# Kernel optimization log

Measured on AMD Instinct MI355X. Metric: run time of the kernel, lower is better.

The kernel has to match this reference:

```python
import jax, jax.numpy as jnp
import numpy as np

S, B, D, H, L = 512, 64, 512, 512, 2


def setup_inputs() -> dict:
    key = jax.random.key(0)
    ks = jax.random.split(key, 2 + 4 * L * 2)
    x = jax.random.normal(ks[0], (S, B, D), jnp.float32)
    # ragged lengths -> time-major float mask, as the torch module expects
    lengths = jax.random.randint(ks[1], (B,), S // 2, S + 1)
    mask = (jnp.arange(S)[:, None] < lengths[None, :]).astype(jnp.float32)
    inp = {"x": x, "mask": mask}
    s = 1.0 / np.sqrt(H)  # torch RNNCell default init scale
    ki = 2
    for l in range(L):
        in_dim = D if l == 0 else 2 * H
        for d in ("f", "b"):
            k1, k2, k3, k4 = jax.random.split(ks[ki], 4)
            ki += 1
            inp[f"Wih{l}{d}"] = jax.random.uniform(k1, (4 * H, in_dim), jnp.float32, -s, s)
            inp[f"Whh{l}{d}"] = jax.random.uniform(k2, (4 * H, H), jnp.float32, -s, s)
            inp[f"bih{l}{d}"] = jax.random.uniform(k3, (4 * H,), jnp.float32, -s, s)
            inp[f"bhh{l}{d}"] = jax.random.uniform(k4, (4 * H,), jnp.float32, -s, s)
    return inp


def _run_lstm(x, mask, Wih, Whh, bih, bhh, reverse):
    # x: [S,B,in], mask: [S,B]. init hidden is zeros (init_hidden=None path),
    # so the mask blend h*m + h0*(1-m) reduces to h*m.
    b = x.shape[1]
    h0 = jnp.zeros((b, H), x.dtype)

    def step(carry, inp):
        xt, mt = inp
        h, c = carry
        gates = xt @ Wih.T + bih + h @ Whh.T + bhh  # [B, 4H]
        i, f, g, o = jnp.split(gates, 4, axis=-1)
        c2 = jax.nn.sigmoid(f) * c + jax.nn.sigmoid(i) * jnp.tanh(g)
        h2 = jax.nn.sigmoid(o) * jnp.tanh(c2)
        m = mt[:, None]
        h2 = h2 * m
        c2 = c2 * m
        return (h2, c2), h2

    (hn, cn), out = jax.lax.scan(step, (h0, h0), (x, mask), reverse=reverse)
    return out, hn, cn


def reference(x, mask,
              Wih0f, Whh0f, bih0f, bhh0f, Wih0b, Whh0b, bih0b, bhh0b,
              Wih1f, Whh1f, bih1f, bhh1f, Wih1b, Whh1b, bih1b, bhh1b):
    layers = [((Wih0f, Whh0f, bih0f, bhh0f), (Wih0b, Whh0b, bih0b, bhh0b)),
              ((Wih1f, Whh1f, bih1f, bhh1f), (Wih1b, Whh1b, bih1b, bhh1b))]
    h = x
    hn, cn = [], []
    for pf, pb in layers:
        of, hf, cf = _run_lstm(h, mask, *pf, reverse=False)
        ob, hb, cb = _run_lstm(h, mask, *pb, reverse=True)
        h = jnp.concatenate([of, ob], axis=2)  # [S,B,2H]
        hn.append(jnp.concatenate([hf, hb], axis=1))
        cn.append(jnp.concatenate([cf, cb], axis=1))
    return h, (jnp.stack(hn, axis=0), jnp.stack(cn, axis=0))
```

## Files before the change

### kernel.cpp

```cpp
#include <hip/hip_runtime.h>
#include <hip/hip_bf16.h>
#include <stdint.h>

#define S_LEN 512
#define BATCH 64
#define DDIM  512
#define HID   512
#define SB    32768

typedef __attribute__((ext_vector_type(8))) short bf16x8;
typedef __attribute__((ext_vector_type(4))) short short4v;
typedef __attribute__((ext_vector_type(4))) float f32x4;

struct __align__(128) Bar { unsigned cnt; unsigned gen; };

__device__ __forceinline__ float bf2f(short s) {
  return __uint_as_float(((unsigned)(unsigned short)s) << 16);
}

__device__ __forceinline__ void gload_lds16(const void* g, void* l) {
  __builtin_amdgcn_global_load_lds(
      (const __attribute__((address_space(1))) void*)g,
      (__attribute__((address_space(3))) void*)l, 16, 0, 0);
}


__global__ void k_f32_to_bf16(const float* __restrict__ src,
                              __hip_bfloat16* __restrict__ dst, int n) {
  int i = (blockIdx.x * blockDim.x + threadIdx.x) * 8;
  if (i >= n) return;
  float4 a = *(const float4*)(src + i);
  float4 b = *(const float4*)(src + i + 4);
  __hip_bfloat16 t[8];
  t[0] = __float2bfloat16(a.x); t[1] = __float2bfloat16(a.y);
  t[2] = __float2bfloat16(a.z); t[3] = __float2bfloat16(a.w);
  t[4] = __float2bfloat16(b.x); t[5] = __float2bfloat16(b.y);
  t[6] = __float2bfloat16(b.z); t[7] = __float2bfloat16(b.w);
  *(bf16x8*)(dst + i) = *(bf16x8*)t;
}

__global__ void k_permW(const float* __restrict__ src,
                        __hip_bfloat16* __restrict__ dst, int K) {
  int idx = blockIdx.x * 256 + threadIdx.x;
  int p = idx / K, k = idx - p * K;
  int g = p & 3, j = p >> 2;
  dst[idx] = __float2bfloat16(src[(size_t)(g * HID + j) * K + k]);
}

__global__ void k_permB(const float* __restrict__ bih, const float* __restrict__ bhh,
                        float* __restrict__ dst) {
  int p = blockIdx.x * 256 + threadIdx.x;
  int g = p & 3, j = p >> 2;
  dst[p] = bih[g * HID + j] + bhh[g * HID + j];
}

__global__ __launch_bounds__(256) void k_gemm_in(
    const __hip_bfloat16* __restrict__ A,
    const __hip_bfloat16* __restrict__ W,
    const float* __restrict__ bsumL,
    __hip_bfloat16* __restrict__ G,
    int K) {
  __shared__ uint4 lds4[2048];
  char* ldsA = (char*)lds4;
  char* ldsB = (char*)lds4 + 16384;
  int tid = threadIdx.x, lane = tid & 63, wid = tid >> 6;
  int wm = wid >> 1, wn = wid & 1;
  int bm = blockIdx.x, by = blockIdx.y;
  int lr = lane & 15, lk = lane >> 4;
  f32x4 acc[4][4] = {};
  const char* gA = (const char*)A;
  const char* gW = (const char*)W;
  for (int kk = 0; kk < K; kk += 64) {
    #pragma unroll
    for (int i = 0; i < 4; i++) {
      int ch = i * 256 + tid;
      int row = ch >> 3, c16 = ch & 7;
      gload_lds16(gA + (size_t)(bm * 128 + row) * (K * 2) + kk * 2 + c16 * 16,
                  ldsA + (i * 256 + wid * 64) * 16);
      gload_lds16(gW + (size_t)(by * 128 + row) * (K * 2) + kk * 2 + c16 * 16,
                  ldsB + (i * 256 + wid * 64) * 16);
    }
    __syncthreads();
    #pragma unroll
    for (int ks = 0; ks < 2; ks++) {
      bf16x8 af[4], bfr[4];
      #pragma unroll
      for (int mi = 0; mi < 4; mi++) {
        int r = wm * 64 + mi * 16 + lr;
        af[mi] = *(const bf16x8*)(ldsA + r * 128 + ks * 64 + lk * 16);
      }
      #pragma unroll
      for (int ni = 0; ni < 4; ni++) {
        int r = wn * 64 + ni * 16 + lr;
        bfr[ni] = *(const bf16x8*)(ldsB + r * 128 + ks * 64 + lk * 16);
      }
      #pragma unroll
      for (int mi = 0; mi < 4; mi++)
        #pragma unroll
        for (int ni = 0; ni < 4; ni++)
          acc[mi][ni] = __builtin_amdgcn_mfma_f32_16x16x32_bf16(
              af[mi], bfr[ni], acc[mi][ni], 0, 0, 0);
    }
    __syncthreads();
  }
  #pragma unroll
  for (int ni = 0; ni < 4; ni++) {
    int n = by * 128 + wn * 64 + ni * 16 + lr;
    int d = n >> 11, p = n & 2047;
    float bias = bsumL[d * 2048 + p];
    #pragma unroll
    for (int mi = 0; mi < 4; mi++) {
      int mbase = bm * 128 + wm * 64 + mi * 16 + lk * 4;
      #pragma unroll
      for (int r = 0; r < 4; r++) {
        int m = mbase + r;
        G[((size_t)d * SB + m) * 2048 + p] =
            __float2bfloat16(acc[mi][ni][r] + bias);
      }
    }
  }
}

__global__ __launch_bounds__(512, 1) void k_scan(
    const __hip_bfloat16* __restrict__ G,
    const __hip_bfloat16* __restrict__ Whp,
    __hip_bfloat16* __restrict__ Y,
    const float* __restrict__ mask,
    float* __restrict__ outH,
    float* __restrict__ hn, float* __restrict__ cn,
    Bar* __restrict__ bars) {
  __shared__ char ldsH[65536];
  float* gatesF = (float*)ldsH;
  int tid = threadIdx.x, lane = tid & 63, wid = tid >> 6;
  int bn = blockIdx.x & 31;
  int dir = blockIdx.x >> 5;
  int wm = wid >> 1, wn = wid & 1;
  int lr = lane & 15, lk = lane >> 4;
  int arow = wm * 16 + lr;
  Bar* bar = bars + dir;
  const __hip_bfloat16* Gd = G + (size_t)dir * SB * 2048;

  int cb = tid >> 3, cup = tid & 7;

  bf16x8 bfrag[16][2];
  {
    const __hip_bfloat16* w0 =
        Whp + (size_t)(dir * 2048 + bn * 64 + wn * 32 + lr) * 512;
    #pragma unroll
    for (int ni = 0; ni < 2; ni++)
      #pragma unroll
      for (int ks = 0; ks < 16; ks++)
        bfrag[ks][ni] = *(const bf16x8*)(w0 + (size_t)ni * 16 * 512 + ks * 32 + lk * 8);
  }

  float creg[2] = {0.f, 0.f};

  int t0 = dir ? (S_LEN - 1) : 0;
  bf16x8 gv = *(const bf16x8*)(Gd + ((size_t)t0 * 64 + cb) * 2048 + bn * 64 + cup * 8);

  for (int s = 0; s < S_LEN; ++s) {
    int t = dir ? (S_LEN - 1 - s) : s;
    f32x4 acc[2] = {};
    if (s > 0) {
      int tprev = dir ? t + 1 : t - 1;
      const char* srcH = (const char*)Y + (size_t)tprev * 131072 + dir * 1024;
      uint64_t tH[16];
      #pragma unroll
      for (int i = 0; i < 16; ++i) {
        int ch = i * 512 + tid, row = ch >> 7, c8 = ch & 127;
        tH[i] = __hip_atomic_load(
            (const uint64_t*)(srcH + (size_t)row * 2048 + c8 * 8),
            __ATOMIC_RELAXED, __HIP_MEMORY_SCOPE_AGENT);
      }
      #pragma unroll
      for (int i = 0; i < 16; ++i) {
        int ch = i * 512 + tid, row = ch >> 7, c8 = ch & 127;
        *(uint64_t*)(ldsH + row * 1024 + ((c8 * 8) ^ ((row & 7) << 4))) = tH[i];
      }
      __syncthreads();
      #pragma unroll
      for (int ks = 0; ks < 16; ++ks) {
        bf16x8 a = *(const bf16x8*)(
            ldsH + arow * 1024 + ((ks * 64 + lk * 16) ^ ((arow & 7) << 4)));
        acc[0] = __builtin_amdgcn_mfma_f32_16x16x32_bf16(a, bfrag[ks][0], acc[0], 0, 0, 0);
        acc[1] = __builtin_amdgcn_mfma_f32_16x16x32_bf16(a, bfrag[ks][1], acc[1], 0, 0, 0);
      }
      __syncthreads();
      #pragma unroll
      for (int ni = 0; ni < 2; ++ni)
        #pragma unroll
        for (int r = 0; r < 4; ++r)
          gatesF[(wm * 16 + lk * 4 + r) * 68 + wn * 32 + ni * 16 + lr] = acc[ni][r];
      __syncthreads();
    }

    float m = mask[t * 64 + cb];
    float h2v[2], c2v[2];
    #pragma unroll
    for (int it = 0; it < 2; ++it) {
      int u = cup * 2 + it;
      float gi = 0.f, gf = 0.f, gg = 0.f, go = 0.f;
      if (s > 0) {
        gi = gatesF[cb * 68 + u * 4 + 0];
        gf = gatesF[cb * 68 + u * 4 + 1];
        gg = gatesF[cb * 68 + u * 4 + 2];
        go = gatesF[cb * 68 + u * 4 + 3];
      }
      gi += bf2f(gv[it * 4 + 0]); gf += bf2f(gv[it * 4 + 1]);
      gg += bf2f(gv[it * 4 + 2]); go += bf2f(gv[it * 4 + 3]);
      float si = 1.f / (1.f + __expf(-gi));
      float sf = 1.f / (1.f + __expf(-gf));
      float so = 1.f / (1.f + __expf(-go));
      float tg = 1.f - 2.f / (1.f + __expf(2.f * gg));
      float c2 = sf * creg[it] + si * tg;
      float h2 = so * (1.f - 2.f / (1.f + __expf(2.f * c2)));
      h2 *= m; c2 *= m;
      creg[it] = c2; h2v[it] = h2; c2v[it] = c2;
    }
    {
      __hip_bfloat16 b0 = __float2bfloat16(h2v[0]);
      __hip_bfloat16 b1 = __float2bfloat16(h2v[1]);
      unsigned w = (unsigned)*(unsigned short*)&b0 |
                   ((unsigned)*(unsigned short*)&b1 << 16);
      uint32_t* yw = (uint32_t*)((char*)Y + ((size_t)t * 64 + cb) * 2048 +
                                 dir * 1024 + (bn * 16 + cup * 2) * 2);
      __hip_atomic_store(yw, w, __ATOMIC_RELAXED, __HIP_MEMORY_SCOPE_AGENT);
    }
    if (outH) {
      float2* ow = (float2*)(outH + ((size_t)t * 64 + cb) * 1024 +
                             dir * 512 + bn * 16 + cup * 2);
      *ow = make_float2(h2v[0], h2v[1]);
    }
    if (s == S_LEN - 1) {
      size_t fi = (size_t)cb * 1024 + dir * 512 + bn * 16 + cup * 2;
      hn[fi] = h2v[0]; hn[fi + 1] = h2v[1];
      cn[fi] = c2v[0]; cn[fi + 1] = c2v[1];
    }

    if (s < S_LEN - 1) {
      asm volatile("" ::: "memory");
      int snx = s + 1;
      int tnx = dir ? (S_LEN - 1 - snx) : snx;
      bf16x8 gvn = *(const bf16x8*)(Gd + ((size_t)tnx * 64 + cb) * 2048 +
                                    bn * 64 + cup * 8);
      asm volatile("s_waitcnt vmcnt(1)" ::: "memory");
      __syncthreads();
      if (tid == 0) {
        unsigned prev = __hip_atomic_fetch_add(&bar->cnt, 1u, __ATOMIC_RELAXED,
                                               __HIP_MEMORY_SCOPE_AGENT);
        if ((prev & 31u) == 31u) {
          __hip_atomic_fetch_add(&bar->gen, 1u, __ATOMIC_RELAXED,
                                 __HIP_MEMORY_SCOPE_AGENT);
        } else {
          int guard = 0;
          while (__hip_atomic_load(&bar->gen, __ATOMIC_RELAXED,
                                   __HIP_MEMORY_SCOPE_AGENT) <= (unsigned)s) {
            __builtin_amdgcn_s_sleep(1);
            if (++guard > (1 << 24)) break;
          }
        }
      }
      __syncthreads();
      gv = gvn;
    }
  }
}


extern "C" void kernel_launch(void* const* d_in, const int* in_sizes, int n_in,
                              void* d_out, int out_size, void* d_ws, size_t ws_size,
                              hipStream_t stream) {
  const float* x    = (const float*)d_in[0];
  const float* mask = (const float*)d_in[1];
  const float* Wih[4] = {(const float*)d_in[2], (const float*)d_in[6],
                         (const float*)d_in[10], (const float*)d_in[14]};
  const float* Whh[4] = {(const float*)d_in[3], (const float*)d_in[7],
                         (const float*)d_in[11], (const float*)d_in[15]};
  const float* bih[4] = {(const float*)d_in[4], (const float*)d_in[8],
                         (const float*)d_in[12], (const float*)d_in[16]};
  const float* bhh[4] = {(const float*)d_in[5], (const float*)d_in[9],
                         (const float*)d_in[13], (const float*)d_in[17]};

  char* ws = (char*)d_ws;
  Bar*            bars  = (Bar*)ws;
  __hip_bfloat16* Xbf   = (__hip_bfloat16*)(ws + 4096);
  __hip_bfloat16* Y0    = (__hip_bfloat16*)(ws + 33558528);
  __hip_bfloat16* Y1    = (__hip_bfloat16*)(ws + 100667392);
  __hip_bfloat16* WpIh0 = (__hip_bfloat16*)(ws + 167776256);
  __hip_bfloat16* WpIh1 = (__hip_bfloat16*)(ws + 171970560);
  __hip_bfloat16* WpHh  = (__hip_bfloat16*)(ws + 180359168);
  float*          bsum  = (float*)(ws + 188747776);
  __hip_bfloat16* Gbuf  = (__hip_bfloat16*)(ws + 188780544);

  float* out = (float*)d_out;
  float* hn = out + (size_t)S_LEN * BATCH * 1024;
  float* cn = hn + 2 * BATCH * 1024;

  hipMemsetAsync(bars, 0, 4 * sizeof(Bar), stream);

  k_f32_to_bf16<<<8192, 256, 0, stream>>>(x, Xbf, SB * DDIM);
  for (int ld = 0; ld < 4; ld++) {
    int K = (ld < 2) ? 512 : 1024;
    __hip_bfloat16* dst = (ld < 2) ? (WpIh0 + (size_t)ld * 2048 * 512)
                                   : (WpIh1 + (size_t)(ld - 2) * 2048 * 1024);
    k_permW<<<(2048 * K) / 256, 256, 0, stream>>>(Wih[ld], dst, K);
    k_permW<<<(2048 * 512) / 256, 256, 0, stream>>>(Whh[ld], WpHh + (size_t)ld * 2048 * 512, 512);
    k_permB<<<8, 256, 0, stream>>>(bih[ld], bhh[ld], bsum + ld * 2048);
  }

  k_gemm_in<<<dim3(256, 32), 256, 0, stream>>>(Xbf, WpIh0, bsum, Gbuf, 512);
  k_scan<<<64, 512, 0, stream>>>(Gbuf, WpHh, Y0, mask, nullptr, hn, cn, bars);
  k_gemm_in<<<dim3(256, 32), 256, 0, stream>>>(Y0, WpIh1, bsum + 2 * 2048, Gbuf, 1024);
  k_scan<<<64, 512, 0, stream>>>(Gbuf, WpHh + (size_t)2 * 2048 * 512, Y1, mask,
                                 out, hn + 2 * BATCH * 512, cn + 2 * BATCH * 512,
                                 bars + 2);
}
```

Measured before the change: 5.977 ms.

## Replace grid barrier with sentinel-polling dataflow sync on hidden-state buffer

Removes the per-step global atomic counter barrier between the 32 workgroups of each direction. Instead, the Y buffers are pre-filled with a 0xFFFF bf16 sentinel (a NaN pattern), and each workgroup spins on reading the previous timestep's hidden state until no sentinel values remain. This lets blocks proceed as soon as their own data is ready. It also gives gatesF its own LDS array so one __syncthreads can go, and prefetches the next mask value. The costs are two extra 64MB memsets per call and reliance on h never encoding exactly 0xFFFF. There is also a risk of reading stale or partial values, since the polling has no release/acquire ordering.

```diff
diff --git a/kernel.cpp b/kernel.cpp
--- a/kernel.cpp
+++ b/kernel.cpp
@@ -9,10 +9,7 @@
 #define SB    32768
 
 typedef __attribute__((ext_vector_type(8))) short bf16x8;
-typedef __attribute__((ext_vector_type(4))) short short4v;
 typedef __attribute__((ext_vector_type(4))) float f32x4;
-
-struct __align__(128) Bar { unsigned cnt; unsigned gen; };
 
 __device__ __forceinline__ float bf2f(short s) {
   return __uint_as_float(((unsigned)(unsigned short)s) << 16);
@@ -127,17 +124,15 @@
     __hip_bfloat16* __restrict__ Y,
     const float* __restrict__ mask,
     float* __restrict__ outH,
-    float* __restrict__ hn, float* __restrict__ cn,
-    Bar* __restrict__ bars) {
+    float* __restrict__ hn, float* __restrict__ cn) {
   __shared__ char ldsH[65536];
-  float* gatesF = (float*)ldsH;
+  __shared__ float gatesF[64 * 68];
   int tid = threadIdx.x, lane = tid & 63, wid = tid >> 6;
   int bn = blockIdx.x & 31;
   int dir = blockIdx.x >> 5;
   int wm = wid >> 1, wn = wid & 1;
   int lr = lane & 15, lk = lane >> 4;
   int arow = wm * 16 + lr;
-  Bar* bar = bars + dir;
   const __hip_bfloat16* Gd = G + (size_t)dir * SB * 2048;
 
   int cb = tid >> 3, cup = tid & 7;
@@ -157,6 +152,7 @@
 
   int t0 = dir ? (S_LEN - 1) : 0;
   bf16x8 gv = *(const bf16x8*)(Gd + ((size_t)t0 * 64 + cb) * 2048 + bn * 64 + cup * 8);
+  float mreg = mask[t0 * 64 + cb];
 
   for (int s = 0; s < S_LEN; ++s) {
     int t = dir ? (S_LEN - 1 - s) : s;
@@ -165,12 +161,25 @@
       int tprev = dir ? t + 1 : t - 1;
       const char* srcH = (const char*)Y + (size_t)tprev * 131072 + dir * 1024;
       uint64_t tH[16];
-      #pragma unroll
-      for (int i = 0; i < 16; ++i) {
-        int ch = i * 512 + tid, row = ch >> 7, c8 = ch & 127;
-        tH[i] = __hip_atomic_load(
-            (const uint64_t*)(srcH + (size_t)row * 2048 + c8 * 8),
-            __ATOMIC_RELAXED, __HIP_MEMORY_SCOPE_AGENT);
+      int guard = 0;
+      for (;;) {
+        #pragma unroll
+        for (int i = 0; i < 16; ++i) {
+          int ch = i * 512 + tid, row = ch >> 7, c8 = ch & 127;
+          tH[i] = __hip_atomic_load(
+              (const uint64_t*)(srcH + (size_t)row * 2048 + c8 * 8),
+              __ATOMIC_RELAXED, __HIP_MEMORY_SCOPE_AGENT);
+        }
+        unsigned long long bad = 0;
+        #pragma unroll
+        for (int i = 0; i < 16; ++i) {
+          uint64_t v = tH[i];
+          bad |= ((v & 0xFFFFull) == 0xFFFFull);
+          bad |= (((v >> 32) & 0xFFFFull) == 0xFFFFull);
+        }
+        if (!bad) break;
+        __builtin_amdgcn_s_sleep(1);
+        if (++guard > (1 << 14)) break;
       }
       #pragma unroll
       for (int i = 0; i < 16; ++i) {
@@ -185,7 +194,6 @@
         acc[0] = __builtin_amdgcn_mfma_f32_16x16x32_bf16(a, bfrag[ks][0], acc[0], 0, 0, 0);
         acc[1] = __builtin_amdgcn_mfma_f32_16x16x32_bf16(a, bfrag[ks][1], acc[1], 0, 0, 0);
       }
-      __syncthreads();
       #pragma unroll
       for (int ni = 0; ni < 2; ++ni)
         #pragma unroll
@@ -194,7 +202,6 @@
       __syncthreads();
     }
 
-    float m = mask[t * 64 + cb];
     float h2v[2], c2v[2];
     #pragma unroll
     for (int it = 0; it < 2; ++it) {
@@ -214,7 +221,7 @@
       float tg = 1.f - 2.f / (1.f + __expf(2.f * gg));
       float c2 = sf * creg[it] + si * tg;
       float h2 = so * (1.f - 2.f / (1.f + __expf(2.f * c2)));
-      h2 *= m; c2 *= m;
+      h2 *= mreg; c2 *= mreg;
       creg[it] = c2; h2v[it] = h2; c2v[it] = c2;
     }
     {
@@ -239,29 +246,9 @@
 
     if (s < S_LEN - 1) {
       asm volatile("" ::: "memory");
-      int snx = s + 1;
-      int tnx = dir ? (S_LEN - 1 - snx) : snx;
-      bf16x8 gvn = *(const bf16x8*)(Gd + ((size_t)tnx * 64 + cb) * 2048 +
-                                    bn * 64 + cup * 8);
-      asm volatile("s_waitcnt vmcnt(1)" ::: "memory");
-      __syncthreads();
-      if (tid == 0) {
-        unsigned prev = __hip_atomic_fetch_add(&bar->cnt, 1u, __ATOMIC_RELAXED,
-                                               __HIP_MEMORY_SCOPE_AGENT);
-        if ((prev & 31u) == 31u) {
-          __hip_atomic_fetch_add(&bar->gen, 1u, __ATOMIC_RELAXED,
-                                 __HIP_MEMORY_SCOPE_AGENT);
-        } else {
-          int guard = 0;
-          while (__hip_atomic_load(&bar->gen, __ATOMIC_RELAXED,
-                                   __HIP_MEMORY_SCOPE_AGENT) <= (unsigned)s) {
-            __builtin_amdgcn_s_sleep(1);
-            if (++guard > (1 << 24)) break;
-          }
-        }
-      }
-      __syncthreads();
-      gv = gvn;
+      int tnx = dir ? (t - 1) : (t + 1);
+      gv = *(const bf16x8*)(Gd + ((size_t)tnx * 64 + cb) * 2048 + bn * 64 + cup * 8);
+      mreg = mask[tnx * 64 + cb];
     }
   }
 }
@@ -282,21 +269,21 @@
                          (const float*)d_in[13], (const float*)d_in[17]};
 
   char* ws = (char*)d_ws;
-  Bar*            bars  = (Bar*)ws;
-  __hip_bfloat16* Xbf   = (__hip_bfloat16*)(ws + 4096);
-  __hip_bfloat16* Y0    = (__hip_bfloat16*)(ws + 33558528);
-  __hip_bfloat16* Y1    = (__hip_bfloat16*)(ws + 100667392);
-  __hip_bfloat16* WpIh0 = (__hip_bfloat16*)(ws + 167776256);
-  __hip_bfloat16* WpIh1 = (__hip_bfloat16*)(ws + 171970560);
-  __hip_bfloat16* WpHh  = (__hip_bfloat16*)(ws + 180359168);
-  float*          bsum  = (float*)(ws + 188747776);
-  __hip_bfloat16* Gbuf  = (__hip_bfloat16*)(ws + 188780544);
+  __hip_bfloat16* Xbf   = (__hip_bfloat16*)(ws);
+  __hip_bfloat16* Y0    = (__hip_bfloat16*)(ws + 33554432);
+  __hip_bfloat16* Y1    = (__hip_bfloat16*)(ws + 100663296);
+  __hip_bfloat16* WpIh0 = (__hip_bfloat16*)(ws + 167772160);
+  __hip_bfloat16* WpIh1 = (__hip_bfloat16*)(ws + 171966464);
+  __hip_bfloat16* WpHh  = (__hip_bfloat16*)(ws + 180355072);
+  float*          bsum  = (float*)(ws + 188743680);
+  __hip_bfloat16* Gbuf  = (__hip_bfloat16*)(ws + 188776448);
 
   float* out = (float*)d_out;
   float* hn = out + (size_t)S_LEN * BATCH * 1024;
   float* cn = hn + 2 * BATCH * 1024;
 
-  hipMemsetAsync(bars, 0, 4 * sizeof(Bar), stream);
+  hipMemsetAsync(Y0, 0xFF, (size_t)SB * 1024 * 2, stream);
+  hipMemsetAsync(Y1, 0xFF, (size_t)SB * 1024 * 2, stream);
 
   k_f32_to_bf16<<<8192, 256, 0, stream>>>(x, Xbf, SB * DDIM);
   for (int ld = 0; ld < 4; ld++) {
@@ -309,9 +296,8 @@
   }
 
   k_gemm_in<<<dim3(256, 32), 256, 0, stream>>>(Xbf, WpIh0, bsum, Gbuf, 512);
-  k_scan<<<64, 512, 0, stream>>>(Gbuf, WpHh, Y0, mask, nullptr, hn, cn, bars);
+  k_scan<<<64, 512, 0, stream>>>(Gbuf, WpHh, Y0, mask, nullptr, hn, cn);
   k_gemm_in<<<dim3(256, 32), 256, 0, stream>>>(Y0, WpIh1, bsum + 2 * 2048, Gbuf, 1024);
   k_scan<<<64, 512, 0, stream>>>(Gbuf, WpHh + (size_t)2 * 2048 * 512, Y1, mask,
-                                 out, hn + 2 * BATCH * 512, cn + 2 * BATCH * 512,
-                                 bars + 2);
-}
+                                 out, hn + 2 * BATCH * 512, cn + 2 * BATCH * 512);
+}
```

Result: faster. 4.869 ms (-18.5%).
